# Optimization experiments

Hardware: AMD Instinct MI355X
Metric: run time of the kernel (lower is better)

The kernel has to match this reference:

```python
import jax, jax.numpy as jnp
import numpy as np

N, C, W = 64, 64, 4096
F, WW = 64, 9

def next_power2(n):
    return int(2 ** np.ceil(np.log2(n)))

def setup_inputs() -> dict:
    key = jax.random.key(0)
    k1, k2, k3 = jax.random.split(key, 3)
    x = jax.random.normal(k1, (N, C, W), dtype=jnp.float32)
    filt = jax.random.normal(k2, (F, C, WW), dtype=jnp.float32)
    bias = jax.random.normal(k3, (F,), dtype=jnp.float32)
    return {"x": x, "filt": filt, "bias": bias}

def reference(x, filt, bias):
    # FFT-based valid cross-correlation, no spectral compression
    # (preserve_energy_rate=None, index_back=None, out_size=None, padding=None).
    n_, c_, w_ = x.shape
    f_, _, ww_ = filt.shape
    out_W = w_ - ww_ + 1  # valid correlation output length
    fftsize = next_power2(w_ + ww_ - 1)
    xf = jnp.fft.rfft(x, n=fftsize)            # [N, C, K] complex64
    wf = jnp.fft.rfft(filt, n=fftsize)         # [F, C, K] complex64
    # correlation = ifft(Xf * conj(Wf)); sum over channels in freq domain
    of = jnp.einsum('nck,fck->nfk', xf, jnp.conj(wf))  # [N, F, K]
    out = jnp.fft.irfft(of, n=fftsize)[..., :out_W]    # [N, F, out_W] float32
    # original adds bias[f] once per channel iteration -> C * bias
    out = out + (c_ * bias)[None, :, None]
    return out
```

## Files before the change

kernel.cpp:

```cpp
#include <hip/hip_runtime.h>
#include <stdint.h>

#define N_   64
#define C_   64
#define W_   4096
#define F_   64
#define WW_  9
#define OW_  4088
#define WBLK 128
#define WROWS 136

typedef __bf16 bf16x8 __attribute__((ext_vector_type(8)));
typedef float  f32x4  __attribute__((ext_vector_type(4)));

__device__ __forceinline__ unsigned short f2bf(float f) {
    union { float f; uint32_t u; } v; v.f = f;
    uint32_t u = v.u;
    return (unsigned short)((u + 0x7FFFu + ((u >> 16) & 1u)) >> 16);
}

__device__ __forceinline__ uint2 pk4(float a, float b, float c, float d) {
    uint2 r;
    asm volatile("v_cvt_pk_bf16_f32 %0, %1, %2" : "=v"(r.x) : "v"(a), "v"(b));
    asm volatile("v_cvt_pk_bf16_f32 %0, %1, %2" : "=v"(r.y) : "v"(c), "v"(d));
    return r;
}

__global__ __launch_bounds__(256) void prep_filt_k(const float* __restrict__ filt,
                                                   unsigned short* __restrict__ filtB) {
    int id = blockIdx.x * 256 + threadIdx.x;
    if (id < WW_ * F_ * C_) {
        int j    = id & 7;
        int lane = (id >> 3) & 63;
        int u    = (id >> 9) & 1;
        int m    = (id >> 10) & 1;
        int f0h  = (id >> 11) & 1;
        int t    = id >> 12;
        int l15  = lane & 15, lg = lane >> 4;
        int f = f0h * 32 + u * 16 + l15;
        int c = m * 32 + lg * 8 + j;
        filtB[id] = f2bf(filt[(f * C_ + c) * WW_ + t]);
    }
}

__global__ __launch_bounds__(256, 6) void conv_k(const float* __restrict__ x,
                                                 const unsigned short* __restrict__ filtB,
                                                 const float* __restrict__ bias,
                                                 float* __restrict__ out) {
    __shared__ unsigned short xs[WROWS * 64];

    const int tid  = threadIdx.x;
    const int lane = tid & 63;
    const int wv   = tid >> 6;
    const int n    = blockIdx.y;
    const int w0   = blockIdx.x * WBLK;

    {
        const int c4 = (wv << 4) + (((tid >> 4) & 3) << 2);
        const int wq = (tid & 15) << 2;
        const int cg = c4 >> 3;
        const int cs = c4 & 7;
        const float* xb = x + ((size_t)(n * C_ + c4)) * W_ + w0;
        #pragma unroll
        for (int j = 0; j < 2; ++j) {
            const int wl = wq + j * 64;
            float4 r0 = *reinterpret_cast<const float4*>(xb + 0 * W_ + wl);
            float4 r1 = *reinterpret_cast<const float4*>(xb + 1 * W_ + wl);
            float4 r2 = *reinterpret_cast<const float4*>(xb + 2 * W_ + wl);
            float4 r3 = *reinterpret_cast<const float4*>(xb + 3 * W_ + wl);
            const float* p0 = &r0.x; const float* p1 = &r1.x;
            const float* p2 = &r2.x; const float* p3 = &r3.x;
            #pragma unroll
            for (int jj = 0; jj < 4; ++jj) {
                int w = wl + jj;
                uint2 u2 = pk4(p0[jj], p1[jj], p2[jj], p3[jj]);
                *reinterpret_cast<uint2*>(&xs[w * 64 + ((cg ^ (w & 7)) << 3) + cs]) = u2;
            }
        }
        if (tid < 32) {
            const int hc4 = (tid & 15) << 2;
            const int hwl = 128 + ((tid >> 4) << 2);
            const int hcg = hc4 >> 3;
            const int hcs = hc4 & 7;
            #pragma unroll
            for (int jj = 0; jj < 4; ++jj) {
                int w  = hwl + jj;
                int gw = w0 + w;
                float a0 = 0.f, a1 = 0.f, a2 = 0.f, a3 = 0.f;
                if (gw < W_) {
                    const float* hp = x + ((size_t)(n * C_ + hc4)) * W_ + gw;
                    a0 = hp[0];
                    a1 = hp[(size_t)W_];
                    a2 = hp[(size_t)2 * W_];
                    a3 = hp[(size_t)3 * W_];
                }
                uint2 u2 = pk4(a0, a1, a2, a3);
                *reinterpret_cast<uint2*>(&xs[w * 64 + ((hcg ^ (w & 7)) << 3) + hcs]) = u2;
            }
        }
    }
    __syncthreads();

    const int f0h = wv & 1;
    const int whb = (wv >> 1) * 64;
    const int l15 = lane & 15;
    const int lg  = lane >> 4;

    const unsigned short* Bb = filtB + f0h * 2048 + lane * 8;
    const float bv0 = 64.0f * bias[f0h * 32 + l15];
    const float bv1 = 64.0f * bias[f0h * 32 + 16 + l15];

    f32x4 acc[4][2];
    #pragma unroll
    for (int s = 0; s < 4; ++s) {
        acc[s][0] = (f32x4){0.f, 0.f, 0.f, 0.f};
        acc[s][1] = (f32x4){0.f, 0.f, 0.f, 0.f};
    }

    #pragma unroll
    for (int t = 0; t < WW_; ++t) {
        #pragma unroll
        for (int m = 0; m < 2; ++m) {
            bf16x8 b0 = *reinterpret_cast<const bf16x8*>(Bb + t * 4096 + m * 1024);
            bf16x8 b1 = *reinterpret_cast<const bf16x8*>(Bb + t * 4096 + m * 1024 + 512);
            #pragma unroll
            for (int s = 0; s < 4; ++s) {
                int row   = whb + s * 16 + l15 + t;
                int chunk = ((m << 2) | lg) ^ (row & 7);
                bf16x8 a  = *reinterpret_cast<const bf16x8*>(&xs[row * 64 + chunk * 8]);
                acc[s][0] = __builtin_amdgcn_mfma_f32_16x16x32_bf16(a, b0, acc[s][0], 0, 0, 0);
                acc[s][1] = __builtin_amdgcn_mfma_f32_16x16x32_bf16(a, b1, acc[s][1], 0, 0, 0);
            }
        }
    }

    const int fb = f0h * 32 + l15;
    #pragma unroll
    for (int s = 0; s < 4; ++s) {
        int wg = w0 + whb + s * 16 + lg * 4;
        if (wg < OW_) {
            float4 o0, o1;
            o0.x = acc[s][0][0] + bv0; o0.y = acc[s][0][1] + bv0;
            o0.z = acc[s][0][2] + bv0; o0.w = acc[s][0][3] + bv0;
            o1.x = acc[s][1][0] + bv1; o1.y = acc[s][1][1] + bv1;
            o1.z = acc[s][1][2] + bv1; o1.w = acc[s][1][3] + bv1;
            *reinterpret_cast<float4*>(out + ((size_t)(n * F_ + fb) * OW_ + wg))      = o0;
            *reinterpret_cast<float4*>(out + ((size_t)(n * F_ + fb + 16) * OW_ + wg)) = o1;
        }
    }
}

extern "C" void kernel_launch(void* const* d_in, const int* in_sizes, int n_in,
                              void* d_out, int out_size, void* d_ws, size_t ws_size,
                              hipStream_t stream) {
    const float* x    = (const float*)d_in[0];
    const float* filt = (const float*)d_in[1];
    const float* bias = (const float*)d_in[2];
    float* out        = (float*)d_out;

    unsigned short* filtB = (unsigned short*)d_ws;

    prep_filt_k<<<(WW_ * F_ * C_ + 255) / 256, 256, 0, stream>>>(filt, filtB);

    dim3 grid(W_ / WBLK, N_);
    conv_k<<<grid, 256, 0, stream>>>(x, filtB, bias, out);
}
```

Measured before the change: 44.12 us.

## Warp-specialize conv kernel with producer waves double-buffering input tiles

Each block now handles four consecutive width tiles with 512 threads. Four producer waves stage the next tile into a second LDS buffer while four consumer waves run MFMA on the current one, with a barrier between iterations. The goal is to hide global load and bf16 conversion latency behind compute. In exchange the grid has four times fewer blocks, each holding twice the LDS, and half the waves never issue MFMA, which can cut parallelism and occupancy.

```diff
diff --git a/kernel.cpp b/kernel.cpp
--- a/kernel.cpp
+++ b/kernel.cpp
@@ -9,6 +9,7 @@
 #define OW_  4088
 #define WBLK 128
 #define WROWS 136
+#define TPB  4
 
 typedef __bf16 bf16x8 __attribute__((ext_vector_type(8)));
 typedef float  f32x4  __attribute__((ext_vector_type(4)));
@@ -43,110 +44,126 @@
     }
 }
 
-__global__ __launch_bounds__(256, 6) void conv_k(const float* __restrict__ x,
+__global__ __launch_bounds__(512, 4) void conv_k(const float* __restrict__ x,
                                                  const unsigned short* __restrict__ filtB,
                                                  const float* __restrict__ bias,
                                                  float* __restrict__ out) {
-    __shared__ unsigned short xs[WROWS * 64];
+    __shared__ unsigned short xs[2][WROWS * 64];
 
-    const int tid  = threadIdx.x;
-    const int lane = tid & 63;
-    const int wv   = tid >> 6;
-    const int n    = blockIdx.y;
-    const int w0   = blockIdx.x * WBLK;
+    const int tid   = threadIdx.x;
+    const int n     = blockIdx.y;
+    const int wbase = blockIdx.x * (WBLK * TPB);
+    const bool producer = (tid >= 256);
 
-    {
-        const int c4 = (wv << 4) + (((tid >> 4) & 3) << 2);
-        const int wq = (tid & 15) << 2;
-        const int cg = c4 >> 3;
-        const int cs = c4 & 7;
-        const float* xb = x + ((size_t)(n * C_ + c4)) * W_ + w0;
+    const int p   = tid & 255;
+    const int pwv = p >> 6;
+    const int c4  = (pwv << 4) + (((p >> 4) & 3) << 2);
+    const int wq  = (p & 15) << 2;
+    const int cg  = c4 >> 3;
+    const int cs  = c4 & 7;
+    const float* xb = x + ((size_t)(n * C_ + c4)) * W_;
+    const int hc4 = (p & 15) << 2;
+    const int hwl = 128 + ((p >> 4) << 2);
+    const int hcg = hc4 >> 3;
+    const int hcs = hc4 & 7;
+    const float* hb = x + ((size_t)(n * C_ + hc4)) * W_;
+
+    auto STAGE = [&](int b, int w0) {
+        unsigned short* dst = xs[b];
         #pragma unroll
         for (int j = 0; j < 2; ++j) {
             const int wl = wq + j * 64;
-            float4 r0 = *reinterpret_cast<const float4*>(xb + 0 * W_ + wl);
-            float4 r1 = *reinterpret_cast<const float4*>(xb + 1 * W_ + wl);
-            float4 r2 = *reinterpret_cast<const float4*>(xb + 2 * W_ + wl);
-            float4 r3 = *reinterpret_cast<const float4*>(xb + 3 * W_ + wl);
+            float4 r0 = *reinterpret_cast<const float4*>(xb + 0 * W_ + w0 + wl);
+            float4 r1 = *reinterpret_cast<const float4*>(xb + 1 * W_ + w0 + wl);
+            float4 r2 = *reinterpret_cast<const float4*>(xb + 2 * W_ + w0 + wl);
+            float4 r3 = *reinterpret_cast<const float4*>(xb + 3 * W_ + w0 + wl);
             const float* p0 = &r0.x; const float* p1 = &r1.x;
             const float* p2 = &r2.x; const float* p3 = &r3.x;
             #pragma unroll
             for (int jj = 0; jj < 4; ++jj) {
                 int w = wl + jj;
                 uint2 u2 = pk4(p0[jj], p1[jj], p2[jj], p3[jj]);
-                *reinterpret_cast<uint2*>(&xs[w * 64 + ((cg ^ (w & 7)) << 3) + cs]) = u2;
+                *reinterpret_cast<uint2*>(&dst[w * 64 + ((cg ^ (w & 7)) << 3) + cs]) = u2;
             }
         }
-        if (tid < 32) {
-            const int hc4 = (tid & 15) << 2;
-            const int hwl = 128 + ((tid >> 4) << 2);
-            const int hcg = hc4 >> 3;
-            const int hcs = hc4 & 7;
+        if (p < 32) {
             #pragma unroll
             for (int jj = 0; jj < 4; ++jj) {
                 int w  = hwl + jj;
                 int gw = w0 + w;
                 float a0 = 0.f, a1 = 0.f, a2 = 0.f, a3 = 0.f;
                 if (gw < W_) {
-                    const float* hp = x + ((size_t)(n * C_ + hc4)) * W_ + gw;
-                    a0 = hp[0];
-                    a1 = hp[(size_t)W_];
-                    a2 = hp[(size_t)2 * W_];
-                    a3 = hp[(size_t)3 * W_];
+                    a0 = hb[gw];
+                    a1 = hb[gw + (size_t)W_];
+                    a2 = hb[gw + (size_t)2 * W_];
+                    a3 = hb[gw + (size_t)3 * W_];
                 }
                 uint2 u2 = pk4(a0, a1, a2, a3);
-                *reinterpret_cast<uint2*>(&xs[w * 64 + ((hcg ^ (w & 7)) << 3) + hcs]) = u2;
+                *reinterpret_cast<uint2*>(&dst[w * 64 + ((hcg ^ (w & 7)) << 3) + hcs]) = u2;
             }
         }
-    }
-    __syncthreads();
+    };
 
-    const int f0h = wv & 1;
-    const int whb = (wv >> 1) * 64;
-    const int l15 = lane & 15;
-    const int lg  = lane >> 4;
-
+    const int lane = tid & 63;
+    const int wv   = (tid >> 6) & 3;
+    const int f0h  = wv & 1;
+    const int whb  = (wv >> 1) * 64;
+    const int l15  = lane & 15;
+    const int lg   = lane >> 4;
     const unsigned short* Bb = filtB + f0h * 2048 + lane * 8;
     const float bv0 = 64.0f * bias[f0h * 32 + l15];
     const float bv1 = 64.0f * bias[f0h * 32 + 16 + l15];
 
-    f32x4 acc[4][2];
-    #pragma unroll
-    for (int s = 0; s < 4; ++s) {
-        acc[s][0] = (f32x4){0.f, 0.f, 0.f, 0.f};
-        acc[s][1] = (f32x4){0.f, 0.f, 0.f, 0.f};
-    }
-
-    #pragma unroll
-    for (int t = 0; t < WW_; ++t) {
+    auto COMPUTE = [&](int b, int w0) {
+        const unsigned short* src = xs[b];
+        f32x4 acc[4][2];
         #pragma unroll
-        for (int m = 0; m < 2; ++m) {
-            bf16x8 b0 = *reinterpret_cast<const bf16x8*>(Bb + t * 4096 + m * 1024);
-            bf16x8 b1 = *reinterpret_cast<const bf16x8*>(Bb + t * 4096 + m * 1024 + 512);
+        for (int s = 0; s < 4; ++s) {
+            acc[s][0] = (f32x4){0.f, 0.f, 0.f, 0.f};
+            acc[s][1] = (f32x4){0.f, 0.f, 0.f, 0.f};
+        }
+        #pragma unroll
+        for (int t = 0; t < WW_; ++t) {
             #pragma unroll
-            for (int s = 0; s < 4; ++s) {
-                int row   = whb + s * 16 + l15 + t;
-                int chunk = ((m << 2) | lg) ^ (row & 7);
-                bf16x8 a  = *reinterpret_cast<const bf16x8*>(&xs[row * 64 + chunk * 8]);
-                acc[s][0] = __builtin_amdgcn_mfma_f32_16x16x32_bf16(a, b0, acc[s][0], 0, 0, 0);
-                acc[s][1] = __builtin_amdgcn_mfma_f32_16x16x32_bf16(a, b1, acc[s][1], 0, 0, 0);
+            for (int m = 0; m < 2; ++m) {
+                bf16x8 b0 = *reinterpret_cast<const bf16x8*>(Bb + t * 4096 + m * 1024);
+                bf16x8 b1 = *reinterpret_cast<const bf16x8*>(Bb + t * 4096 + m * 1024 + 512);
+                #pragma unroll
+                for (int s = 0; s < 4; ++s) {
+                    int row   = whb + s * 16 + l15 + t;
+                    int chunk = ((m << 2) | lg) ^ (row & 7);
+                    bf16x8 a  = *reinterpret_cast<const bf16x8*>(&src[row * 64 + chunk * 8]);
+                    acc[s][0] = __builtin_amdgcn_mfma_f32_16x16x32_bf16(a, b0, acc[s][0], 0, 0, 0);
+                    acc[s][1] = __builtin_amdgcn_mfma_f32_16x16x32_bf16(a, b1, acc[s][1], 0, 0, 0);
+                }
             }
         }
-    }
+        const int fb = f0h * 32 + l15;
+        #pragma unroll
+        for (int s = 0; s < 4; ++s) {
+            int wg = w0 + whb + s * 16 + lg * 4;
+            if (wg < OW_) {
+                float4 o0, o1;
+                o0.x = acc[s][0][0] + bv0; o0.y = acc[s][0][1] + bv0;
+                o0.z = acc[s][0][2] + bv0; o0.w = acc[s][0][3] + bv0;
+                o1.x = acc[s][1][0] + bv1; o1.y = acc[s][1][1] + bv1;
+                o1.z = acc[s][1][2] + bv1; o1.w = acc[s][1][3] + bv1;
+                *reinterpret_cast<float4*>(out + ((size_t)(n * F_ + fb) * OW_ + wg))      = o0;
+                *reinterpret_cast<float4*>(out + ((size_t)(n * F_ + fb + 16) * OW_ + wg)) = o1;
+            }
+        }
+    };
 
-    const int fb = f0h * 32 + l15;
-    #pragma unroll
-    for (int s = 0; s < 4; ++s) {
-        int wg = w0 + whb + s * 16 + lg * 4;
-        if (wg < OW_) {
-            float4 o0, o1;
-            o0.x = acc[s][0][0] + bv0; o0.y = acc[s][0][1] + bv0;
-            o0.z = acc[s][0][2] + bv0; o0.w = acc[s][0][3] + bv0;
-            o1.x = acc[s][1][0] + bv1; o1.y = acc[s][1][1] + bv1;
-            o1.z = acc[s][1][2] + bv1; o1.w = acc[s][1][3] + bv1;
-            *reinterpret_cast<float4*>(out + ((size_t)(n * F_ + fb) * OW_ + wg))      = o0;
-            *reinterpret_cast<float4*>(out + ((size_t)(n * F_ + fb + 16) * OW_ + wg)) = o1;
+    if (producer) STAGE(0, wbase);
+    __syncthreads();
+    #pragma unroll 1
+    for (int i = 0; i < TPB; ++i) {
+        if (producer) {
+            if (i + 1 < TPB) STAGE((i + 1) & 1, wbase + (i + 1) * WBLK);
+        } else {
+            COMPUTE(i & 1, wbase + i * WBLK);
         }
+        __syncthreads();
     }
 }
 
@@ -162,6 +179,6 @@
 
     prep_filt_k<<<(WW_ * F_ * C_ + 255) / 256, 256, 0, stream>>>(filt, filtB);
 
-    dim3 grid(W_ / WBLK, N_);
-    conv_k<<<grid, 256, 0, stream>>>(x, filtB, bias, out);
+    dim3 grid(W_ / (WBLK * TPB), N_);
+    conv_k<<<grid, 512, 0, stream>>>(x, filtB, bias, out);
 }
```

New measurement: 81.50 us. 84.7% more time.
